# Kernel tuning notes

Measured on AMD Instinct MI355X. Metric: run time of the kernel, lower is better.

Reference implementation:

```python
import jax, jax.numpy as jnp
import numpy as np

B, T, C = 1, 4096, 1024
H = 16
D = C // H  # 64
LN_EPS = 1e-5


def layer_norm(x, g, b):
    mu = jnp.mean(x, axis=-1, keepdims=True)
    var = jnp.mean(jnp.square(x - mu), axis=-1, keepdims=True)
    return (x - mu) * jax.lax.rsqrt(var + LN_EPS) * g + b


def setup_inputs() -> dict:
    key = jax.random.key(0)
    ks = jax.random.split(key, 8)
    s = 0.02
    return {
        "x": jax.random.normal(ks[0], (B, T, C), dtype=jnp.float32),
        "ln1_g": jnp.ones((C,), jnp.float32),
        "ln1_b": jnp.zeros((C,), jnp.float32),
        "Wqkv": jax.random.normal(ks[1], (C, 3 * C), dtype=jnp.float32) * s,
        "bqkv": jnp.zeros((3 * C,), jnp.float32),
        "Wo": jax.random.normal(ks[2], (C, C), dtype=jnp.float32) * s,
        "bo": jnp.zeros((C,), jnp.float32),
        "ln2_g": jnp.ones((C,), jnp.float32),
        "ln2_b": jnp.zeros((C,), jnp.float32),
        "W1": jax.random.normal(ks[3], (C, 4 * C), dtype=jnp.float32) * s,
        "b1": jnp.zeros((4 * C,), jnp.float32),
        "W2": jax.random.normal(ks[4], (4 * C, C), dtype=jnp.float32) * s,
        "b2": jnp.zeros((C,), jnp.float32),
    }


def reference(x, ln1_g, ln1_b, Wqkv, bqkv, Wo, bo, ln2_g, ln2_b, W1, b1, W2, b2):
    b, t, c = x.shape
    x_norm = layer_norm(x, ln1_g, ln1_b)
    qkv = x_norm @ Wqkv + bqkv                      # [B,T,3C]
    qkv = qkv.reshape(b, t, 3, H, D).transpose(2, 0, 3, 1, 4)  # [3,B,H,T,D]
    Q, K, V = qkv[0], qkv[1], qkv[2]
    scores = jnp.einsum("bhtd,bhsd->bhts", Q, K) / jnp.sqrt(jnp.float32(D))
    causal = jnp.tril(jnp.ones((t, t), dtype=bool))  # [T,T]
    scores = jnp.where(causal[None, None], scores, -jnp.inf)
    weights = jax.nn.softmax(scores, axis=-1)
    attn = jnp.einsum("bhts,bhsd->bhtd", weights, V)  # [B,H,T,D]
    attn = attn.transpose(0, 2, 1, 3).reshape(b, t, c)
    x = x + (attn @ Wo + bo)
    h = layer_norm(x, ln2_g, ln2_b)
    h = jax.nn.gelu(h @ W1 + b1, approximate=False) @ W2 + b2
    return x + h
```

## Files before the change

kernel.cpp:

```cpp
#include <hip/hip_runtime.h>
#include <math.h>

typedef __bf16 bf16_t;
typedef __attribute__((ext_vector_type(8))) __bf16 bf16x8;
typedef __attribute__((ext_vector_type(4))) __bf16 bf16x4;
typedef __attribute__((ext_vector_type(4))) float f32x4;
typedef __attribute__((ext_vector_type(16))) float f32x16;
typedef __attribute__((ext_vector_type(4))) unsigned int u32x4;

#define T_LEN 4096
#define C_DIM 1024
#define NH 16
#define HD 64

__device__ __forceinline__ void gload_lds16(const void* g, void* l) {
    __builtin_amdgcn_global_load_lds(
        (__attribute__((address_space(1))) void*)(g),
        (__attribute__((address_space(3))) void*)(l), 16, 0, 0);
}

__device__ __forceinline__ f32x4 mfma16(bf16x8 a, bf16x8 b, f32x4 c) {
    return __builtin_amdgcn_mfma_f32_16x16x32_bf16(a, b, c, 0, 0, 0);
}

__device__ __forceinline__ f32x16 mfma32(bf16x8 a, bf16x8 b, f32x16 c) {
    return __builtin_amdgcn_mfma_f32_32x32x16_bf16(a, b, c, 0, 0, 0);
}

__device__ __forceinline__ float gelu_exact(float v) {
    return 0.5f * v * (1.0f + erff(v * 0.7071067811865476f));
}

__device__ __forceinline__ void make_frags2(const f32x16 s, bf16x8& fx, bf16x8& fy) {
    unsigned a0, a1, b0, b1;
    asm("v_cvt_pk_bf16_f32 %0, %1, %2" : "=v"(a0) : "v"(s[0]), "v"(s[1]));
    asm("v_cvt_pk_bf16_f32 %0, %1, %2" : "=v"(a1) : "v"(s[2]), "v"(s[3]));
    asm("v_cvt_pk_bf16_f32 %0, %1, %2" : "=v"(b0) : "v"(s[4]), "v"(s[5]));
    asm("v_cvt_pk_bf16_f32 %0, %1, %2" : "=v"(b1) : "v"(s[6]), "v"(s[7]));
    asm("v_permlane32_swap_b32 %0, %1" : "+v"(a0), "+v"(b0));
    asm("v_permlane32_swap_b32 %0, %1" : "+v"(a1), "+v"(b1));
    u32x4 wa = {a0, a1, b0, b1};
    fx = __builtin_bit_cast(bf16x8, wa);
    unsigned c0, c1, d0, d1;
    asm("v_cvt_pk_bf16_f32 %0, %1, %2" : "=v"(c0) : "v"(s[8]), "v"(s[9]));
    asm("v_cvt_pk_bf16_f32 %0, %1, %2" : "=v"(c1) : "v"(s[10]), "v"(s[11]));
    asm("v_cvt_pk_bf16_f32 %0, %1, %2" : "=v"(d0) : "v"(s[12]), "v"(s[13]));
    asm("v_cvt_pk_bf16_f32 %0, %1, %2" : "=v"(d1) : "v"(s[14]), "v"(s[15]));
    asm("v_permlane32_swap_b32 %0, %1" : "+v"(c0), "+v"(d0));
    asm("v_permlane32_swap_b32 %0, %1" : "+v"(c1), "+v"(d1));
    u32x4 wb = {c0, c1, d0, d1};
    fy = __builtin_bit_cast(bf16x8, wb);
}

__global__ __launch_bounds__(256) void transpose_w(
    const float* __restrict__ in, bf16_t* __restrict__ out, int R, int C)
{
    __shared__ float tile[32][33];
    const int tx = threadIdx.x, ty = threadIdx.y;
    const int c0 = blockIdx.x * 32, r0 = blockIdx.y * 32;
#pragma unroll
    for (int j = 0; j < 4; ++j)
        tile[ty + j * 8][tx] = in[(size_t)(r0 + ty + j * 8) * C + c0 + tx];
    __syncthreads();
#pragma unroll
    for (int j = 0; j < 4; ++j)
        out[(size_t)(c0 + ty + j * 8) * R + r0 + tx] = (bf16_t)tile[tx][ty + j * 8];
}

__global__ __launch_bounds__(256) void vtrans(
    const bf16_t* __restrict__ qkv, bf16_t* __restrict__ vt)
{
    __shared__ bf16_t tile[32][33];
    const int tx = threadIdx.x, ty = threadIdx.y;
    const int h = blockIdx.z;
    const int t0 = blockIdx.x * 32, d0 = blockIdx.y * 32;
#pragma unroll
    for (int j = 0; j < 4; ++j)
        tile[ty + j * 8][tx] =
            qkv[(size_t)(t0 + ty + j * 8) * 3072 + 2048 + h * 64 + d0 + tx];
    __syncthreads();
#pragma unroll
    for (int j = 0; j < 4; ++j)
        vt[(size_t)h * (64 * 4096) + (size_t)(d0 + ty + j * 8) * 4096 + t0 + tx] =
            tile[tx][ty + j * 8];
}

__global__ __launch_bounds__(256) void ln_bf16(
    const float* __restrict__ x, const float* __restrict__ gam,
    const float* __restrict__ bet, bf16_t* __restrict__ out)
{
    const int row = blockIdx.x, t = threadIdx.x;
    const float4 v = *(const float4*)(x + (size_t)row * 1024 + t * 4);
    float s1 = v.x + v.y + v.z + v.w;
    float s2 = v.x * v.x + v.y * v.y + v.z * v.z + v.w * v.w;
#pragma unroll
    for (int m = 1; m < 64; m <<= 1) {
        s1 += __shfl_xor(s1, m);
        s2 += __shfl_xor(s2, m);
    }
    __shared__ float red[8];
    if ((t & 63) == 0) { red[(t >> 6) * 2] = s1; red[(t >> 6) * 2 + 1] = s2; }
    __syncthreads();
    s1 = red[0] + red[2] + red[4] + red[6];
    s2 = red[1] + red[3] + red[5] + red[7];
    const float mu = s1 * (1.0f / 1024.0f);
    const float inv = rsqrtf(s2 * (1.0f / 1024.0f) - mu * mu + 1e-5f);
    const float4 gg = *(const float4*)(gam + t * 4);
    const float4 bb = *(const float4*)(bet + t * 4);
    bf16x4 o;
    o[0] = (bf16_t)((v.x - mu) * inv * gg.x + bb.x);
    o[1] = (bf16_t)((v.y - mu) * inv * gg.y + bb.y);
    o[2] = (bf16_t)((v.z - mu) * inv * gg.z + bb.z);
    o[3] = (bf16_t)((v.w - mu) * inv * gg.w + bb.w);
    *(bf16x4*)(out + (size_t)row * 1024 + t * 4) = o;
}

template <int EPI>
__global__ __launch_bounds__(256, 2) void gemm_bt(
    const bf16_t* __restrict__ A, const bf16_t* __restrict__ Bt,
    const float* __restrict__ bias, const float* __restrict__ res,
    bf16_t* __restrict__ outb, float* __restrict__ outf,
    int M, int N, int Klen, int Kstr)
{
    __shared__ alignas(1024) bf16_t Alds[4][128 * 32];
    __shared__ alignas(1024) bf16_t Blds[4][128 * 32];
    const int t = threadIdx.x;
    const int lane = t & 63, w = t >> 6;
    const int wr = w >> 1, wc = w & 1;
    const int g = lane >> 4, ci = lane & 15;

    int bx, by, chunk = 0;
    if constexpr (EPI == 3) {
        const int flat = blockIdx.x + 8 * blockIdx.y;
        const int xcd = flat & 7, s = flat >> 3;
        chunk = s >> 5;
        const int s2 = s & 31;
        by = xcd * 4 + (s2 >> 3);
        bx = s2 & 7;
        A  += (size_t)chunk * Klen;
        Bt += (size_t)chunk * Klen;
    } else {
        const int NB = gridDim.x, MB = gridDim.y;
        const int flat = blockIdx.x + NB * blockIdx.y;
        const int xcd = flat & 7, slot = flat >> 3;
        by = xcd * (MB >> 3) + slot / NB;
        bx = slot % NB;
    }
    const int m0 = by * 128, n0 = bx * 128;

    f32x4 acc[4][4];
#pragma unroll
    for (int i = 0; i < 4; ++i)
#pragma unroll
        for (int j = 0; j < 4; ++j)
#pragma unroll
            for (int k = 0; k < 4; ++k) acc[i][j][k] = 0.0f;

    const int r0 = t >> 2;
    const int cc = (t & 3) * 8;
    const int nkt = Klen >> 5;

    auto stage = [&](int kt) {
        const int b = kt & 3;
        const int kk = kt * 32;
        char* aB = (char*)&Alds[b][0] + w * 1024;
        char* bB = (char*)&Blds[b][0] + w * 1024;
        gload_lds16(A + (size_t)(m0 + r0) * Kstr + kk + cc, aB);
        gload_lds16(A + (size_t)(m0 + r0 + 64) * Kstr + kk + cc, aB + 4096);
        gload_lds16(Bt + (size_t)(n0 + r0) * Kstr + kk + cc, bB);
        gload_lds16(Bt + (size_t)(n0 + r0 + 64) * Kstr + kk + cc, bB + 4096);
    };

    stage(0);
    if (nkt > 1) stage(1);
    for (int kt = 0; kt < nkt; ++kt) {
        if (kt + 2 < nkt) {
            stage(kt + 2);
            asm volatile("s_waitcnt vmcnt(8)" ::: "memory");
        } else if (kt + 1 < nkt) {
            asm volatile("s_waitcnt vmcnt(4)" ::: "memory");
        } else {
            asm volatile("s_waitcnt vmcnt(0)" ::: "memory");
        }
        __builtin_amdgcn_s_barrier();
        __builtin_amdgcn_sched_barrier(0);
        const int b = kt & 3;
        const bf16_t* ap = &Alds[b][0] + (wr * 64 + ci) * 32 + g * 8;
        const bf16_t* bp = &Blds[b][0] + (wc * 64 + ci) * 32 + g * 8;
        bf16x8 af[4], bf[4];
#pragma unroll
        for (int mt = 0; mt < 4; ++mt) af[mt] = *(const bf16x8*)(ap + mt * 16 * 32);
#pragma unroll
        for (int nt = 0; nt < 4; ++nt) bf[nt] = *(const bf16x8*)(bp + nt * 16 * 32);
        __builtin_amdgcn_s_setprio(1);
#pragma unroll
        for (int mt = 0; mt < 4; ++mt)
#pragma unroll
            for (int nt = 0; nt < 4; ++nt)
                acc[mt][nt] = mfma16(af[mt], bf[nt], acc[mt][nt]);
        __builtin_amdgcn_s_setprio(0);
    }

#pragma unroll
    for (int nt = 0; nt < 4; ++nt) {
        const int col = n0 + wc * 64 + nt * 16 + ci;
        const float bv = (EPI == 3) ? 0.0f : bias[col];
#pragma unroll
        for (int mt = 0; mt < 4; ++mt) {
            const int row = m0 + wr * 64 + mt * 16 + g * 4;
#pragma unroll
            for (int r = 0; r < 4; ++r) {
                float v = acc[mt][nt][r] + bv;
                if constexpr (EPI == 1) v = gelu_exact(v);
                if constexpr (EPI == 2) {
                    outf[(size_t)(row + r) * N + col] =
                        v + res[(size_t)(row + r) * N + col];
                } else if constexpr (EPI == 3) {
                    outf[((size_t)chunk * M + row + r) * N + col] = v;
                } else {
                    outb[(size_t)(row + r) * N + col] = (bf16_t)v;
                }
            }
        }
    }
}

__global__ __launch_bounds__(256) void w2_combine(
    const float* __restrict__ part, const float* __restrict__ bias,
    const float* __restrict__ res, float* __restrict__ out)
{
    const int row = blockIdx.x, t = threadIdx.x;
    const int c = t * 4;
    const float4 a = *(const float4*)(part + (size_t)row * 1024 + c);
    const float4 b = *(const float4*)(part + ((size_t)T_LEN + row) * 1024 + c);
    const float4 rr = *(const float4*)(res + (size_t)row * 1024 + c);
    const float4 bb = *(const float4*)(bias + c);
    float4 o;
    o.x = a.x + b.x + rr.x + bb.x;
    o.y = a.y + b.y + rr.y + bb.y;
    o.z = a.z + b.z + rr.z + bb.z;
    o.w = a.w + b.w + rr.w + bb.w;
    *(float4*)(out + (size_t)row * 1024 + c) = o;
}

template <int EPI>
__global__ __launch_bounds__(512, 2) void gemm256(
    const bf16_t* __restrict__ A, const bf16_t* __restrict__ Bt,
    const float* __restrict__ bias, bf16_t* __restrict__ outb,
    int M, int N, int K)
{
    __shared__ alignas(1024) bf16_t lds[2][2][256 * 64];
    const int t = threadIdx.x, lane = t & 63, w = t >> 6;
    const int g = lane >> 4, ci = lane & 15;
    const int wr = w >> 2, wc = w & 3;
    const int NB = gridDim.x;
    const int nwg = NB * gridDim.y;
    const int flat = blockIdx.x + NB * blockIdx.y;
    const int rix = (flat & 7) * (nwg >> 3) + (flat >> 3);
    const int m0 = (rix / NB) * 256, n0 = (rix % NB) * 256;
    const int NKT = K >> 6;

    f32x4 acc[8][4];
#pragma unroll
    for (int i = 0; i < 8; ++i)
#pragma unroll
        for (int j = 0; j < 4; ++j)
#pragma unroll
            for (int k2 = 0; k2 < 4; ++k2) acc[i][j][k2] = 0.0f;

    const int sw0 = (g ^ (ci & 7)) * 8;
    const int sw1 = ((4 + g) ^ (ci & 7)) * 8;

    auto stage = [&](int h, int ktile, int b) {
#pragma unroll
        for (int i = 0; i < 2; ++i) {
            const int idx = i * 512 + t;
            const int r = idx >> 3;
            const int c = (t & 7) ^ (r & 7);
            const bf16_t* src = ((h < 2) ? A : Bt)
                + (size_t)(((h < 2) ? m0 : n0) + (h & 1) * 128 + r) * K
                + ktile * 64 + c * 8;
            bf16_t* dst = &lds[b][h >> 1][(h & 1) * 8192] + (i * 512 + w * 64) * 8;
            gload_lds16(src, dst);
        }
    };

    bf16x8 a[4][2], b2[2][2][2];

    stage(0, 0, 0); stage(3, 0, 0); stage(1, 0, 0); stage(2, 0, 0);
    if (NKT > 1) { stage(0, 1, 1); stage(3, 1, 1); stage(1, 1, 1); }
    asm volatile("s_waitcnt vmcnt(6)" ::: "memory");
    __builtin_amdgcn_s_barrier();

    for (int kt = 0; kt < NKT; ++kt) {
        const int cur = kt & 1;
        const bf16_t* Ab = &lds[cur][0][0];
        const bf16_t* Bb = &lds[cur][1][0];

#pragma unroll
        for (int mi = 0; mi < 4; ++mi) {
            const bf16_t* ap = Ab + (wr * 64 + mi * 16 + ci) * 64;
            a[mi][0] = *(const bf16x8*)(ap + sw0);
            a[mi][1] = *(const bf16x8*)(ap + sw1);
        }
#pragma unroll
        for (int ni = 0; ni < 2; ++ni) {
            const bf16_t* bp = Bb + (wc * 32 + ni * 16 + ci) * 64;
            b2[0][ni][0] = *(const bf16x8*)(bp + sw0);
            b2[0][ni][1] = *(const bf16x8*)(bp + sw1);
        }
        if (kt + 1 < NKT) stage(2, kt + 1, cur ^ 1);
        __builtin_amdgcn_s_barrier();
        asm volatile("s_waitcnt lgkmcnt(0)" ::: "memory");
        __builtin_amdgcn_sched_barrier(0);
        __builtin_amdgcn_s_setprio(1);
#pragma unroll
        for (int mi = 0; mi < 4; ++mi)
#pragma unroll
            for (int ni = 0; ni < 2; ++ni) {
                acc[mi][ni] = mfma16(a[mi][0], b2[0][ni][0], acc[mi][ni]);
                acc[mi][ni] = mfma16(a[mi][1], b2[0][ni][1], acc[mi][ni]);
            }
        __builtin_amdgcn_s_setprio(0);
        __builtin_amdgcn_s_barrier();

#pragma unroll
        for (int ni = 0; ni < 2; ++ni) {
            const bf16_t* bp = Bb + (128 + wc * 32 + ni * 16 + ci) * 64;
            b2[1][ni][0] = *(const bf16x8*)(bp + sw0);
            b2[1][ni][1] = *(const bf16x8*)(bp + sw1);
        }
        if (kt + 2 < NKT) stage(0, kt + 2, cur);
        __builtin_amdgcn_s_barrier();
        asm volatile("s_waitcnt lgkmcnt(0)" ::: "memory");
        __builtin_amdgcn_sched_barrier(0);
        __builtin_amdgcn_s_setprio(1);
#pragma unroll
        for (int mi = 0; mi < 4; ++mi)
#pragma unroll
            for (int ni = 0; ni < 2; ++ni) {
                acc[mi][2 + ni] = mfma16(a[mi][0], b2[1][ni][0], acc[mi][2 + ni]);
                acc[mi][2 + ni] = mfma16(a[mi][1], b2[1][ni][1], acc[mi][2 + ni]);
            }
        __builtin_amdgcn_s_setprio(0);
        __builtin_amdgcn_s_barrier();

#pragma unroll
        for (int mi = 0; mi < 4; ++mi) {
            const bf16_t* ap = Ab + (128 + wr * 64 + mi * 16 + ci) * 64;
            a[mi][0] = *(const bf16x8*)(ap + sw0);
            a[mi][1] = *(const bf16x8*)(ap + sw1);
        }
        if (kt + 2 < NKT) stage(3, kt + 2, cur);
        __builtin_amdgcn_s_barrier();
        asm volatile("s_waitcnt lgkmcnt(0)" ::: "memory");
        __builtin_amdgcn_sched_barrier(0);
        __builtin_amdgcn_s_setprio(1);
#pragma unroll
        for (int mi = 0; mi < 4; ++mi)
#pragma unroll
            for (int ni = 0; ni < 2; ++ni) {
                acc[4 + mi][2 + ni] = mfma16(a[mi][0], b2[1][ni][0], acc[4 + mi][2 + ni]);
                acc[4 + mi][2 + ni] = mfma16(a[mi][1], b2[1][ni][1], acc[4 + mi][2 + ni]);
            }
        __builtin_amdgcn_s_setprio(0);
        __builtin_amdgcn_s_barrier();

        if (kt + 2 < NKT) stage(1, kt + 2, cur);
        __builtin_amdgcn_s_barrier();
        __builtin_amdgcn_s_setprio(1);
#pragma unroll
        for (int mi = 0; mi < 4; ++mi)
#pragma unroll
            for (int ni = 0; ni < 2; ++ni) {
                acc[4 + mi][ni] = mfma16(a[mi][0], b2[0][ni][0], acc[4 + mi][ni]);
                acc[4 + mi][ni] = mfma16(a[mi][1], b2[0][ni][1], acc[4 + mi][ni]);
            }
        __builtin_amdgcn_s_setprio(0);
        if (kt + 2 < NKT) asm volatile("s_waitcnt vmcnt(6)" ::: "memory");
        else              asm volatile("s_waitcnt vmcnt(0)" ::: "memory");
        __builtin_amdgcn_s_barrier();
    }

#pragma unroll
    for (int mrep = 0; mrep < 8; ++mrep) {
        const int row = m0 + (mrep >> 2) * 128 + wr * 64 + (mrep & 3) * 16 + g * 4;
#pragma unroll
        for (int nrep = 0; nrep < 4; ++nrep) {
            const int col = n0 + (nrep >> 1) * 128 + wc * 32 + (nrep & 1) * 16 + ci;
            const float bv = bias[col];
#pragma unroll
            for (int jr = 0; jr < 4; ++jr) {
                float v = acc[mrep][nrep][jr] + bv;
                if constexpr (EPI == 1) v = gelu_exact(v);
                outb[(size_t)(row + jr) * N + col] = (bf16_t)v;
            }
        }
    }
}

__global__ __launch_bounds__(256, 2) void attn_fwd(
    const bf16_t* __restrict__ qkv, const bf16_t* __restrict__ vt,
    float* __restrict__ opart, float* __restrict__ mlbuf)
{
    __shared__ alignas(1024) bf16_t Klds[2][64 * 64];
    __shared__ alignas(1024) bf16_t Vlds[2][64 * 64];
    const int t = threadIdx.x, lane = t & 63, w = t >> 6;
    const int hi = lane >> 5, li = lane & 31;
    const int lq = li >> 2;
    const int h = blockIdx.x;
    const int y = blockIdx.y;
    const int qt = 31 - (y >> 1);
    const int chunk = y & 1;
    const int q0 = qt * 128;
    const int qrow = q0 + w * 32 + li;
    const int wDiag = 2 * qt + (w >> 1);
    const int ktA = chunk ? (qt + 1) : 0;
    const int ktB = chunk ? (2 * qt + 2) : (qt + 1);
    const float C1 = 0.125f * 1.4426950408889634f;

    bf16x8 qf[4];
#pragma unroll
    for (int ks = 0; ks < 4; ++ks)
        qf[ks] = *(const bf16x8*)(qkv + (size_t)qrow * 3072 + h * 64 + ks * 16 + hi * 8);

    f32x16 oacc[2];
#pragma unroll
    for (int d = 0; d < 2; ++d)
#pragma unroll
        for (int r = 0; r < 16; ++r) oacc[d][r] = 0.0f;
    float m_i = -1e30f, l_i = 0.0f;

    const int sr = t >> 3;
    const int sx = ((t & 7) ^ ((sr >> 2) & 7)) * 8;

    auto stageKV = [&](int kt, int b) {
        const size_t kbase = (size_t)(kt * 64) * 3072 + 1024 + h * 64 + sx;
        const size_t vbase = (size_t)h * 262144 + (size_t)kt * 64 + sx;
#pragma unroll
        for (int i = 0; i < 2; ++i) {
            gload_lds16(qkv + kbase + (size_t)(i * 32 + sr) * 3072,
                        (char*)&Klds[b][0] + (size_t)(i * 2048 + t * 8) * 2);
            gload_lds16(vt + vbase + (size_t)(i * 32 + sr) * 4096,
                        (char*)&Vlds[b][0] + (size_t)(i * 2048 + t * 8) * 2);
        }
    };

    stageKV(ktA, 0);
    for (int kt = ktA; kt < ktB; ++kt) {
        const int cur = (kt - ktA) & 1;
        asm volatile("s_waitcnt vmcnt(0)" ::: "memory");
        __syncthreads();
        if (kt + 1 < ktB) stageKV(kt + 1, cur ^ 1);

        if (kt <= wDiag) {
            const bf16_t* Kb = &Klds[cur][0];
            const bf16_t* Vb = &Vlds[cur][0];
            f32x16 s0, s1;
#pragma unroll
            for (int r = 0; r < 16; ++r) { s0[r] = 0.0f; s1[r] = 0.0f; }

            __builtin_amdgcn_s_setprio(1);
#pragma unroll
            for (int ks = 0; ks < 4; ++ks) {
                const int cs = ((ks * 2 + hi) ^ lq) * 8;
                s0 = mfma32(*(const bf16x8*)(Kb + li * 64 + cs), qf[ks], s0);
                s1 = mfma32(*(const bf16x8*)(Kb + (32 + li) * 64 + cs), qf[ks], s1);
            }
            __builtin_amdgcn_s_setprio(0);

            bf16x8 vf[4][2];
#pragma unroll
            for (int ks = 0; ks < 4; ++ks) {
                const int cs = ((ks * 2 + hi) ^ lq) * 8;
                vf[ks][0] = *(const bf16x8*)(Vb + li * 64 + cs);
                vf[ks][1] = *(const bf16x8*)(Vb + (32 + li) * 64 + cs);
            }

            if (kt == wDiag) {
                const int kb0 = kt * 64 + 4 * hi;
#pragma unroll
                for (int r = 0; r < 16; ++r) {
                    const int kp0 = kb0 + (r & 3) + 8 * (r >> 2);
                    if (kp0 > qrow) s0[r] = -1e30f;
                    if (kp0 + 32 > qrow) s1[r] = -1e30f;
                }
            }
            float mt8[8];
#pragma unroll
            for (int r = 0; r < 8; ++r)
                mt8[r] = fmaxf(fmaxf(s0[r], s0[r + 8]), fmaxf(s1[r], s1[r + 8]));
#pragma unroll
            for (int d = 4; d >= 1; d >>= 1)
#pragma unroll
                for (int r = 0; r < d; ++r) mt8[r] = fmaxf(mt8[r], mt8[r + d]);
            float mx = fmaxf(mt8[0], __shfl_xor(mt8[0], 32));
            const float pmax = mx * C1;
            if (!__all(pmax - m_i <= 8.0f)) {
                const float newm = fmaxf(m_i, pmax);
                const float scf = exp2f(m_i - newm);
                m_i = newm;
                l_i *= scf;
#pragma unroll
                for (int r = 0; r < 16; ++r) { oacc[0][r] *= scf; oacc[1][r] *= scf; }
            }
            float st8[8];
#pragma unroll
            for (int r = 0; r < 16; ++r) {
                s0[r] = exp2f(fmaf(s0[r], C1, -m_i));
                s1[r] = exp2f(fmaf(s1[r], C1, -m_i));
            }
#pragma unroll
            for (int r = 0; r < 8; ++r)
                st8[r] = (s0[r] + s0[r + 8]) + (s1[r] + s1[r + 8]);
#pragma unroll
            for (int d = 4; d >= 1; d >>= 1)
#pragma unroll
                for (int r = 0; r < d; ++r) st8[r] += st8[r + d];
            l_i += st8[0] + __shfl_xor(st8[0], 32);

            bf16x8 pf[4];
            make_frags2(s0, pf[0], pf[1]);
            make_frags2(s1, pf[2], pf[3]);

            __builtin_amdgcn_s_setprio(1);
#pragma unroll
            for (int ks = 0; ks < 4; ++ks) {
                oacc[0] = mfma32(vf[ks][0], pf[ks], oacc[0]);
                oacc[1] = mfma32(vf[ks][1], pf[ks], oacc[1]);
            }
            __builtin_amdgcn_s_setprio(0);
        }
        __syncthreads();
    }

    float* op = opart + ((size_t)chunk * T_LEN + qrow) * 1024 + h * 64 + hi * 4;
#pragma unroll
    for (int dblk = 0; dblk < 2; ++dblk)
#pragma unroll
        for (int gi = 0; gi < 4; ++gi) {
            f32x4 o4;
#pragma unroll
            for (int j = 0; j < 4; ++j) o4[j] = oacc[dblk][gi * 4 + j];
            *(f32x4*)(op + dblk * 32 + gi * 8) = o4;
        }
    if (hi == 0) {
        float2 ml = make_float2(m_i, l_i);
        *(float2*)(mlbuf + (((size_t)chunk * T_LEN + qrow) * NH + h) * 2) = ml;
    }
}

__global__ __launch_bounds__(256) void attn_combine(
    const float* __restrict__ opart, const float* __restrict__ mlbuf,
    bf16_t* __restrict__ out)
{
    const int row = blockIdx.x, t = threadIdx.x;
    const int c = t * 4, h = c >> 6;
    const float2 ml0 = *(const float2*)(mlbuf + ((size_t)row * NH + h) * 2);
    const float2 ml1 = *(const float2*)(mlbuf + (((size_t)T_LEN + row) * NH + h) * 2);
    const float M = fmaxf(ml0.x, ml1.x);
    const float w0 = exp2f(ml0.x - M), w1 = exp2f(ml1.x - M);
    const float inv = 1.0f / (ml0.y * w0 + ml1.y * w1);
    const float4 o0 = *(const float4*)(opart + (size_t)row * 1024 + c);
    const float4 o1 = *(const float4*)(opart + ((size_t)T_LEN + row) * 1024 + c);
    bf16x4 o;
    o[0] = (bf16_t)((o0.x * w0 + o1.x * w1) * inv);
    o[1] = (bf16_t)((o0.y * w0 + o1.y * w1) * inv);
    o[2] = (bf16_t)((o0.z * w0 + o1.z * w1) * inv);
    o[3] = (bf16_t)((o0.w * w0 + o1.w * w1) * inv);
    *(bf16x4*)(out + (size_t)row * 1024 + c) = o;
}

extern "C" void kernel_launch(void* const* d_in, const int* in_sizes, int n_in,
                              void* d_out, int out_size, void* d_ws, size_t ws_size,
                              hipStream_t stream)
{
    const float* x    = (const float*)d_in[0];
    const float* ln1g = (const float*)d_in[1];
    const float* ln1b = (const float*)d_in[2];
    const float* Wqkv = (const float*)d_in[3];
    const float* bqkv = (const float*)d_in[4];
    const float* Wo   = (const float*)d_in[5];
    const float* bo   = (const float*)d_in[6];
    const float* ln2g = (const float*)d_in[7];
    const float* ln2b = (const float*)d_in[8];
    const float* W1   = (const float*)d_in[9];
    const float* b1   = (const float*)d_in[10];
    const float* W2   = (const float*)d_in[11];
    const float* b2   = (const float*)d_in[12];
    float* outp = (float*)d_out;

    char* p = (char*)d_ws;
    bf16_t* WqkvT = (bf16_t*)p; p += (size_t)3072 * 1024 * 2;
    bf16_t* WoT   = (bf16_t*)p; p += (size_t)1024 * 1024 * 2;
    bf16_t* W1T   = (bf16_t*)p; p += (size_t)4096 * 1024 * 2;
    bf16_t* W2T   = (bf16_t*)p; p += (size_t)1024 * 4096 * 2;
    bf16_t* xn    = (bf16_t*)p; p += (size_t)4096 * 1024 * 2;
    bf16_t* qkv   = (bf16_t*)p; p += (size_t)4096 * 3072 * 2;
    bf16_t* vtb   = (bf16_t*)p; p += (size_t)16 * 64 * 4096 * 2;
    bf16_t* attnb = (bf16_t*)p; p += (size_t)4096 * 1024 * 2;
    float*  x2    = (float*)p;  p += (size_t)4096 * 1024 * 4;
    bf16_t* hb    = (bf16_t*)p; p += (size_t)4096 * 1024 * 2;
    bf16_t* g1    = (bf16_t*)p; p += (size_t)4096 * 4096 * 2;
    float*  opart = (float*)p;  p += (size_t)2 * 4096 * 1024 * 4;
    float*  mlbuf = (float*)p;  p += (size_t)2 * 4096 * 16 * 2 * 4;
    float*  w2part = opart;

    const dim3 tb(32, 8);
    transpose_w<<<dim3(96, 32),  tb, 0, stream>>>(Wqkv, WqkvT, 1024, 3072);
    transpose_w<<<dim3(32, 32),  tb, 0, stream>>>(Wo,   WoT,   1024, 1024);
    transpose_w<<<dim3(128, 32), tb, 0, stream>>>(W1,   W1T,   1024, 4096);
    transpose_w<<<dim3(32, 128), tb, 0, stream>>>(W2,   W2T,   4096, 1024);

    ln_bf16<<<4096, 256, 0, stream>>>(x, ln1g, ln1b, xn);
    gemm256<0><<<dim3(12, 16), 512, 0, stream>>>(xn, WqkvT, bqkv,
                                                 qkv, 4096, 3072, 1024);
    vtrans<<<dim3(128, 2, 16), tb, 0, stream>>>(qkv, vtb);
    attn_fwd<<<dim3(16, 64), 256, 0, stream>>>(qkv, vtb, opart, mlbuf);
    attn_combine<<<4096, 256, 0, stream>>>(opart, mlbuf, attnb);
    gemm_bt<2><<<dim3(8, 32), 256, 0, stream>>>(attnb, WoT, bo, x,
                                                nullptr, x2, 4096, 1024, 1024, 1024);
    ln_bf16<<<4096, 256, 0, stream>>>(x2, ln2g, ln2b, hb);
    gemm256<1><<<dim3(16, 16), 512, 0, stream>>>(hb, W1T, b1,
                                                 g1, 4096, 4096, 1024);
    gemm_bt<3><<<dim3(8, 64), 256, 0, stream>>>(g1, W2T, nullptr, nullptr,
                                                nullptr, w2part, 4096, 1024, 2048, 4096);
    w2_combine<<<4096, 256, 0, stream>>>(w2part, b2, x2, outp);
}
```

Measured before the change: 272.4 us.

## Merge weight transposes, compute softmax row sums via MFMA, store bf16 attention partials

Merges the four weight-transpose launches into one kernel that picks its matrix from the block index. In attention, the per-row softmax sum is now built by an extra MFMA against a ones vector instead of VALU reductions and shuffles. The partial attention outputs are stored as bf16 rather than fp32, which halves the write and read traffic between attn_fwd and attn_combine. The W2 partial buffer gets its own fp32 allocation. The trade-offs are extra MFMA work per tile and lower precision in the partial outputs.

Result: no change. 267.7 us (-1.7%).

```diff
diff --git a/kernel.cpp b/kernel.cpp
--- a/kernel.cpp
+++ b/kernel.cpp
@@ -52,12 +52,21 @@
     fy = __builtin_bit_cast(bf16x8, wb);
 }
 
-__global__ __launch_bounds__(256) void transpose_w(
-    const float* __restrict__ in, bf16_t* __restrict__ out, int R, int C)
+__global__ __launch_bounds__(256) void transpose_all(
+    const float* __restrict__ wqkv, const float* __restrict__ wo,
+    const float* __restrict__ w1, const float* __restrict__ w2,
+    bf16_t* __restrict__ oqkv, bf16_t* __restrict__ owo,
+    bf16_t* __restrict__ ow1, bf16_t* __restrict__ ow2)
 {
     __shared__ float tile[32][33];
+    int s = blockIdx.x;
+    const float* in; bf16_t* out; int R, C, NBX;
+    if (s < 3072)      {            in = wqkv; out = oqkv; R = 1024; C = 3072; NBX = 96; }
+    else if (s < 4096) { s -= 3072; in = wo;   out = owo;  R = 1024; C = 1024; NBX = 32; }
+    else if (s < 8192) { s -= 4096; in = w1;   out = ow1;  R = 1024; C = 4096; NBX = 128; }
+    else               { s -= 8192; in = w2;   out = ow2;  R = 4096; C = 1024; NBX = 32; }
     const int tx = threadIdx.x, ty = threadIdx.y;
-    const int c0 = blockIdx.x * 32, r0 = blockIdx.y * 32;
+    const int c0 = (s % NBX) * 32, r0 = (s / NBX) * 32;
 #pragma unroll
     for (int j = 0; j < 4; ++j)
         tile[ty + j * 8][tx] = in[(size_t)(r0 + ty + j * 8) * C + c0 + tx];
@@ -401,7 +410,7 @@
 
 __global__ __launch_bounds__(256, 2) void attn_fwd(
     const bf16_t* __restrict__ qkv, const bf16_t* __restrict__ vt,
-    float* __restrict__ opart, float* __restrict__ mlbuf)
+    bf16_t* __restrict__ opart, float* __restrict__ mlbuf)
 {
     __shared__ alignas(1024) bf16_t Klds[2][64 * 64];
     __shared__ alignas(1024) bf16_t Vlds[2][64 * 64];
@@ -423,13 +432,14 @@
 #pragma unroll
     for (int ks = 0; ks < 4; ++ks)
         qf[ks] = *(const bf16x8*)(qkv + (size_t)qrow * 3072 + h * 64 + ks * 16 + hi * 8);
-
-    f32x16 oacc[2];
-#pragma unroll
-    for (int d = 0; d < 2; ++d)
-#pragma unroll
-        for (int r = 0; r < 16; ++r) oacc[d][r] = 0.0f;
-    float m_i = -1e30f, l_i = 0.0f;
+    bf16x8 ones8;
+#pragma unroll
+    for (int j = 0; j < 8; ++j) ones8[j] = (bf16_t)1.0f;
+
+    f32x16 oacc[2], lacc;
+#pragma unroll
+    for (int r = 0; r < 16; ++r) { oacc[0][r] = 0.0f; oacc[1][r] = 0.0f; lacc[r] = 0.0f; }
+    float m_i = -1e30f;
 
     const int sr = t >> 3;
     const int sx = ((t & 7) ^ ((sr >> 2) & 7)) * 8;
@@ -500,24 +510,16 @@
                 const float newm = fmaxf(m_i, pmax);
                 const float scf = exp2f(m_i - newm);
                 m_i = newm;
-                l_i *= scf;
-#pragma unroll
-                for (int r = 0; r < 16; ++r) { oacc[0][r] *= scf; oacc[1][r] *= scf; }
-            }
-            float st8[8];
+#pragma unroll
+                for (int r = 0; r < 16; ++r) {
+                    oacc[0][r] *= scf; oacc[1][r] *= scf; lacc[r] *= scf;
+                }
+            }
 #pragma unroll
             for (int r = 0; r < 16; ++r) {
                 s0[r] = exp2f(fmaf(s0[r], C1, -m_i));
                 s1[r] = exp2f(fmaf(s1[r], C1, -m_i));
             }
-#pragma unroll
-            for (int r = 0; r < 8; ++r)
-                st8[r] = (s0[r] + s0[r + 8]) + (s1[r] + s1[r + 8]);
-#pragma unroll
-            for (int d = 4; d >= 1; d >>= 1)
-#pragma unroll
-                for (int r = 0; r < d; ++r) st8[r] += st8[r + d];
-            l_i += st8[0] + __shfl_xor(st8[0], 32);
 
             bf16x8 pf[4];
             make_frags2(s0, pf[0], pf[1]);
@@ -528,30 +530,31 @@
             for (int ks = 0; ks < 4; ++ks) {
                 oacc[0] = mfma32(vf[ks][0], pf[ks], oacc[0]);
                 oacc[1] = mfma32(vf[ks][1], pf[ks], oacc[1]);
+                lacc    = mfma32(ones8,     pf[ks], lacc);
             }
             __builtin_amdgcn_s_setprio(0);
         }
         __syncthreads();
     }
 
-    float* op = opart + ((size_t)chunk * T_LEN + qrow) * 1024 + h * 64 + hi * 4;
+    bf16_t* op = opart + ((size_t)chunk * T_LEN + qrow) * 1024 + h * 64 + hi * 4;
 #pragma unroll
     for (int dblk = 0; dblk < 2; ++dblk)
 #pragma unroll
         for (int gi = 0; gi < 4; ++gi) {
-            f32x4 o4;
-#pragma unroll
-            for (int j = 0; j < 4; ++j) o4[j] = oacc[dblk][gi * 4 + j];
-            *(f32x4*)(op + dblk * 32 + gi * 8) = o4;
+            bf16x4 o4;
+#pragma unroll
+            for (int j = 0; j < 4; ++j) o4[j] = (bf16_t)oacc[dblk][gi * 4 + j];
+            *(bf16x4*)(op + dblk * 32 + gi * 8) = o4;
         }
     if (hi == 0) {
-        float2 ml = make_float2(m_i, l_i);
+        float2 ml = make_float2(m_i, lacc[0]);
         *(float2*)(mlbuf + (((size_t)chunk * T_LEN + qrow) * NH + h) * 2) = ml;
     }
 }
 
 __global__ __launch_bounds__(256) void attn_combine(
-    const float* __restrict__ opart, const float* __restrict__ mlbuf,
+    const bf16_t* __restrict__ opart, const float* __restrict__ mlbuf,
     bf16_t* __restrict__ out)
 {
     const int row = blockIdx.x, t = threadIdx.x;
@@ -561,13 +564,12 @@
     const float M = fmaxf(ml0.x, ml1.x);
     const float w0 = exp2f(ml0.x - M), w1 = exp2f(ml1.x - M);
     const float inv = 1.0f / (ml0.y * w0 + ml1.y * w1);
-    const float4 o0 = *(const float4*)(opart + (size_t)row * 1024 + c);
-    const float4 o1 = *(const float4*)(opart + ((size_t)T_LEN + row) * 1024 + c);
+    const bf16x4 o0 = *(const bf16x4*)(opart + (size_t)row * 1024 + c);
+    const bf16x4 o1 = *(const bf16x4*)(opart + ((size_t)T_LEN + row) * 1024 + c);
     bf16x4 o;
-    o[0] = (bf16_t)((o0.x * w0 + o1.x * w1) * inv);
-    o[1] = (bf16_t)((o0.y * w0 + o1.y * w1) * inv);
-    o[2] = (bf16_t)((o0.z * w0 + o1.z * w1) * inv);
-    o[3] = (bf16_t)((o0.w * w0 + o1.w * w1) * inv);
+#pragma unroll
+    for (int j = 0; j < 4; ++j)
+        o[j] = (bf16_t)(((float)o0[j] * w0 + (float)o1[j] * w1) * inv);
     *(bf16x4*)(out + (size_t)row * 1024 + c) = o;
 }
 
@@ -602,20 +604,17 @@
     float*  x2    = (float*)p;  p += (size_t)4096 * 1024 * 4;
     bf16_t* hb    = (bf16_t*)p; p += (size_t)4096 * 1024 * 2;
     bf16_t* g1    = (bf16_t*)p; p += (size_t)4096 * 4096 * 2;
-    float*  opart = (float*)p;  p += (size_t)2 * 4096 * 1024 * 4;
+    bf16_t* opart = (bf16_t*)p; p += (size_t)2 * 4096 * 1024 * 2;
     float*  mlbuf = (float*)p;  p += (size_t)2 * 4096 * 16 * 2 * 4;
-    float*  w2part = opart;
-
-    const dim3 tb(32, 8);
-    transpose_w<<<dim3(96, 32),  tb, 0, stream>>>(Wqkv, WqkvT, 1024, 3072);
-    transpose_w<<<dim3(32, 32),  tb, 0, stream>>>(Wo,   WoT,   1024, 1024);
-    transpose_w<<<dim3(128, 32), tb, 0, stream>>>(W1,   W1T,   1024, 4096);
-    transpose_w<<<dim3(32, 128), tb, 0, stream>>>(W2,   W2T,   4096, 1024);
+    float*  w2part = (float*)p; p += (size_t)2 * 4096 * 1024 * 4;
+
+    transpose_all<<<12288, dim3(32, 8), 0, stream>>>(Wqkv, Wo, W1, W2,
+                                                     WqkvT, WoT, W1T, W2T);
 
     ln_bf16<<<4096, 256, 0, stream>>>(x, ln1g, ln1b, xn);
     gemm256<0><<<dim3(12, 16), 512, 0, stream>>>(xn, WqkvT, bqkv,
                                                  qkv, 4096, 3072, 1024);
-    vtrans<<<dim3(128, 2, 16), tb, 0, stream>>>(qkv, vtb);
+    vtrans<<<dim3(128, 2, 16), dim3(32, 8), 0, stream>>>(qkv, vtb);
     attn_fwd<<<dim3(16, 64), 256, 0, stream>>>(qkv, vtb, opart, mlbuf);
     attn_combine<<<4096, 256, 0, stream>>>(opart, mlbuf, attnb);
     gemm_bt<2><<<dim3(8, 32), 256, 0, stream>>>(attnb, WoT, bo, x,
```
